# Kernel tuning notes

Hardware: AMD Instinct MI355X
Metric: run time of the kernel (lower is better)

The kernel has to match this reference:

```python
import jax, jax.numpy as jnp
import numpy as np
from jax.ops import segment_sum

N_NODES = 50000
N_EDGES = 800000
NUM_FEAT = 16
EDGE_DIM = 8
H = 100
L = 2
BN_EPS = 1e-5


def setup_inputs() -> dict:
    key = jax.random.key(0)
    ks = iter(jax.random.split(key, 40))
    def w(shape, scale=0.05):
        return (jax.random.normal(next(ks), shape, dtype=jnp.float32) * scale)
    inp = {
        "x": jax.random.normal(next(ks), (N_NODES, NUM_FEAT), dtype=jnp.float32),
        "edge_index": jax.random.randint(next(ks), (2, N_EDGES), 0, N_NODES, dtype=jnp.int64) if jax.config.jax_enable_x64 else jax.random.randint(next(ks), (2, N_EDGES), 0, N_NODES).astype(jnp.int32),
        "edge_attr": jax.random.normal(next(ks), (N_EDGES, EDGE_DIM), dtype=jnp.float32),
        # embeddings
        "node_w": w((NUM_FEAT, H)), "node_b": w((H,)),
        "edge_w": w((EDGE_DIM, H)), "edge_b": w((H,)),
        # per-layer GINEConv MLP (stacked over layers)
        "conv_w1": w((L, H, H)), "conv_b1": w((L, H)),
        "conv_w2": w((L, H, H)), "conv_b2": w((L, H)),
        # batchnorm affine params
        "bn_gamma": jnp.ones((L, H), dtype=jnp.float32), "bn_beta": jnp.zeros((L, H), dtype=jnp.float32),
        # per-layer edge-update MLP
        "emlp_w1": w((L, 3 * H, H)), "emlp_b1": w((L, H)),
        "emlp_w2": w((L, H, H)), "emlp_b2": w((L, H)),
        # final classifier MLP (3H -> 50 -> 25 -> 2); dropout is identity at eval
        "mlp_w1": w((3 * H, 50)), "mlp_b1": w((50,)),
        "mlp_w2": w((50, 25)), "mlp_b2": w((25,)),
        "mlp_w3": w((25, 2)), "mlp_b3": w((2,)),
    }
    return inp


def reference(x, edge_index, edge_attr,
              node_w, node_b, edge_w, edge_b,
              conv_w1, conv_b1, conv_w2, conv_b2,
              bn_gamma, bn_beta,
              emlp_w1, emlp_b1, emlp_w2, emlp_b2,
              mlp_w1, mlp_b1, mlp_w2, mlp_b2, mlp_w3, mlp_b3):
    src, dst = edge_index[0], edge_index[1]
    n_nodes = x.shape[0]

    h = x @ node_w + node_b          # [N, H]
    e = edge_attr @ edge_w + edge_b  # [E, H]

    for i in range(L):
        # GINEConv: out_i = nn((1+eps)*h_i + sum_{e: dst=i} relu(h_src + e)); eps=0
        msg = jax.nn.relu(h[src] + e)                       # [E, H] gather + combine
        agg = segment_sum(msg, dst, num_segments=n_nodes)   # [N, H] scatter-add
        z = h + agg
        z = jax.nn.relu(z @ conv_w1[i] + conv_b1[i]) @ conv_w2[i] + conv_b2[i]
        # BatchNorm (train mode: batch stats over nodes, biased variance)
        mu = jnp.mean(z, axis=0)
        var = jnp.var(z, axis=0)
        z = (z - mu) * jax.lax.rsqrt(var + BN_EPS) * bn_gamma[i] + bn_beta[i]
        h = (h + jax.nn.relu(z)) * 0.5
        # edge update: e += MLP([h_src, h_dst, e]) / 2
        cat = jnp.concatenate([h[src], h[dst], e], axis=-1)  # [E, 3H]
        upd = jax.nn.relu(cat @ emlp_w1[i] + emlp_b1[i]) @ emlp_w2[i] + emlp_b2[i]
        e = e + upd * 0.5

    # per-edge features: relu([h_src, h_dst]) ++ e  -> [E, 3H]
    feat = jnp.concatenate([jax.nn.relu(jnp.concatenate([h[src], h[dst]], axis=-1)), e], axis=-1)
    out = jax.nn.relu(feat @ mlp_w1 + mlp_b1)
    out = jax.nn.relu(out @ mlp_w2 + mlp_b2)
    return out @ mlp_w3 + mlp_b3  # [E, 2]
```

## Files before the change

kernel.cpp:

```cpp
#include <hip/hip_runtime.h>
#include <hip/hip_bf16.h>

#define N_NODES 50000
#define N_EDGES 800000
#define HDIM 100
#define ESTR 104

typedef _Float16 half8_t __attribute__((ext_vector_type(8)));
typedef float f32x4_t __attribute__((ext_vector_type(4)));

struct FragDesc {
  const float* src; int stride; int K; int N; int outOff; int ksteps; int ntiles;
};
struct PrepArgs {
  FragDesc d[17];
  int prefix[18];
  int ndesc;
};

__global__ void k_prep_frags(PrepArgs args, _Float16* __restrict__ out) {
  int b = blockIdx.x;
  int di = 0;
  while (di + 1 < args.ndesc && b >= args.prefix[di + 1]) di++;
  FragDesc d = args.d[di];
  int local = b - args.prefix[di];
  int t = local / d.ksteps;
  int s = local % d.ksteps;
  int lane = threadIdx.x;
  int col = t * 16 + (lane & 15);
  int kb = s * 32 + (lane >> 4) * 8;
  _Float16* o = out + d.outOff + (size_t)((t * d.ksteps + s) * 64 + lane) * 8;
  #pragma unroll
  for (int i = 0; i < 8; ++i) {
    int k = kb + i;
    float v = (k < d.K && col < d.N) ? d.src[(size_t)k * d.stride + col] : 0.0f;
    o[i] = (_Float16)v;
  }
}

__global__ void k_ws_probe(float* out, float mb) { out[0] = mb; }

__device__ __forceinline__ half8_t h8_zero() {
  half8_t a;
  #pragma unroll
  for (int i = 0; i < 8; ++i) a[i] = (_Float16)0.0f;
  return a;
}

__device__ __forceinline__ int swz_idx(int r, int c) {
  int chunk = (c >> 3) ^ (r & 7);
  return r * 128 + chunk * 8 + (c & 7);
}

template<int MODE>
__device__ __forceinline__ void load_a_node(const float* hp0,
                                            const float* ap0,
                                            int row, int lane, half8_t av[4]) {
  int g = lane >> 4;
  bool rv = (row < N_NODES);
  const float* hp = hp0 + (size_t)row * HDIM;
  const float* ap = ap0 + (size_t)row * HDIM;
  #pragma unroll
  for (int s = 0; s < 4; ++s) {
    int kb = s * 32 + g * 8;
    half8_t a = h8_zero();
    if (rv && kb < HDIM) {
      float f[8];
      #pragma unroll
      for (int i = 0; i < 8; ++i) f[i] = 0.0f;
      if (kb + 8 <= HDIM) {
        float4 v0 = *(const float4*)(hp + kb);
        float4 v1 = *(const float4*)(hp + kb + 4);
        f[0] = v0.x; f[1] = v0.y; f[2] = v0.z; f[3] = v0.w;
        f[4] = v1.x; f[5] = v1.y; f[6] = v1.z; f[7] = v1.w;
        if constexpr (MODE == 2) {
          float4 u0 = *(const float4*)(ap + kb);
          float4 u1 = *(const float4*)(ap + kb + 4);
          f[0] += u0.x; f[1] += u0.y; f[2] += u0.z; f[3] += u0.w;
          f[4] += u1.x; f[5] += u1.y; f[6] += u1.z; f[7] += u1.w;
        }
      } else {
        float4 v0 = *(const float4*)(hp + kb);
        f[0] = v0.x; f[1] = v0.y; f[2] = v0.z; f[3] = v0.w;
        if constexpr (MODE == 2) {
          float4 u0 = *(const float4*)(ap + kb);
          f[0] += u0.x; f[1] += u0.y; f[2] += u0.z; f[3] += u0.w;
        }
      }
      #pragma unroll
      for (int i = 0; i < 8; ++i) {
        float v = f[i];
        if constexpr (MODE == 1) v = fmaxf(v, 0.0f);
        a[i] = (_Float16)v;
      }
    }
    av[s] = a;
  }
}

template<int NT, int KS>
__device__ __forceinline__ void mfma_tiles(const half8_t* av, const _Float16* __restrict__ fb,
                                           int lane, f32x4_t* acc) {
  #pragma unroll
  for (int t = 0; t < NT; ++t) {
    #pragma unroll
    for (int s = 0; s < KS; ++s) {
      half8_t bv = *(const half8_t*)(fb + (size_t)(((t * KS + s) * 64 + lane) << 3));
      acc[t] = __builtin_amdgcn_mfma_f32_16x16x32_f16(av[s], bv, acc[t], 0, 0, 0);
    }
  }
}

template<int KS>
__device__ __forceinline__ void lds_read_a(const _Float16* L, int lane, half8_t* av) {
  int r = lane & 15;
  int g = lane >> 4;
  #pragma unroll
  for (int s = 0; s < KS; ++s) {
    int kb = s * 32 + g * 8;
    av[s] = *(const half8_t*)&L[swz_idx(r, kb)];
  }
}

__global__ void k_embed_h(const float* __restrict__ x, const float* __restrict__ w,
                          const float* __restrict__ bias, float* __restrict__ h) {
  int n = blockIdx.x;
  int j = threadIdx.x;
  if (j >= HDIM) return;
  float acc = bias[j];
  #pragma unroll
  for (int k = 0; k < 16; ++k) acc += x[n * 16 + k] * w[k * HDIM + j];
  h[(size_t)n * HDIM + j] = acc;
}

__global__ void k_embed_e(const float* __restrict__ attr, const float* __restrict__ w,
                          const float* __restrict__ bias, const int* __restrict__ src,
                          const int* __restrict__ dst, const float* __restrict__ h,
                          _Float16* __restrict__ e, float* __restrict__ agg) {
  int tid = threadIdx.x;
  int edge = blockIdx.x * 2 + (tid >> 7);
  int j = tid & 127;
  if (edge >= N_EDGES || j >= ESTR) return;
  float acc = 0.0f;
  if (j < HDIM) {
    acc = bias[j];
    #pragma unroll
    for (int k = 0; k < 8; ++k) acc += attr[edge * 8 + k] * w[k * HDIM + j];
  }
  e[(size_t)edge * ESTR + j] = (_Float16)acc;
  if (j < HDIM) {
    float m = h[(size_t)src[edge] * HDIM + j] + acc;
    if (m > 0.0f) atomicAdd(&agg[(size_t)dst[edge] * HDIM + j], m);
  }
}

__global__ __launch_bounds__(256) void k_node_conv(
    const float* __restrict__ h, const float* agg,
    const _Float16* __restrict__ fb1, const _Float16* __restrict__ fb2,
    const float* __restrict__ b1, const float* __restrict__ b2,
    float* z, float* __restrict__ bn_sum, float* __restrict__ bn_sq) {
  __shared__ __align__(16) _Float16 lds[4][2048];
  int lane = threadIdx.x & 63;
  int wave = threadIdx.x >> 6;
  _Float16* L = lds[wave];
  int mbase = (blockIdx.x * 4 + wave) * 16;

  half8_t av[4];
  load_a_node<2>(h, agg, mbase + (lane & 15), lane, av);
  f32x4_t acc[7];
  #pragma unroll
  for (int t = 0; t < 7; ++t) acc[t] = (f32x4_t){0.f, 0.f, 0.f, 0.f};
  mfma_tiles<7, 4>(av, fb1, lane, acc);

  #pragma unroll
  for (int t = 0; t < 7; ++t) {
    int j = t * 16 + (lane & 15);
    float bias = (j < HDIM) ? b1[j] : 0.0f;
    #pragma unroll
    for (int q = 0; q < 4; ++q) {
      int r = (lane >> 4) * 4 + q;
      float v = fmaxf(acc[t][q] + bias, 0.0f);
      if (j >= HDIM) v = 0.0f;
      L[swz_idx(r, j)] = (_Float16)v;
    }
  }
  {
    int r = lane >> 2; int c0 = 112 + (lane & 3) * 4;
    #pragma unroll
    for (int i = 0; i < 4; ++i) L[swz_idx(r, c0 + i)] = (_Float16)0.0f;
  }
  __builtin_amdgcn_sched_barrier(0);

  half8_t av2[4];
  lds_read_a<4>(L, lane, av2);
  f32x4_t acc2[7];
  #pragma unroll
  for (int t = 0; t < 7; ++t) acc2[t] = (f32x4_t){0.f, 0.f, 0.f, 0.f};
  mfma_tiles<7, 4>(av2, fb2, lane, acc2);
  __builtin_amdgcn_sched_barrier(0);

  #pragma unroll
  for (int t = 0; t < 7; ++t) {
    int j = t * 16 + (lane & 15);
    float bias = (j < HDIM) ? b2[j] : 0.0f;
    float colsum = 0.0f, colsq = 0.0f;
    #pragma unroll
    for (int q = 0; q < 4; ++q) {
      int row = mbase + (lane >> 4) * 4 + q;
      float v = acc2[t][q] + bias;
      bool ok = (row < N_NODES) && (j < HDIM);
      if (ok) z[(size_t)row * HDIM + j] = v;
      float sv = ok ? v : 0.0f;
      colsum += sv; colsq += sv * sv;
    }
    colsum += __shfl_xor(colsum, 16);
    colsum += __shfl_xor(colsum, 32);
    colsq  += __shfl_xor(colsq, 16);
    colsq  += __shfl_xor(colsq, 32);
    if (lane < 16 && j < HDIM) {
      atomicAdd(&bn_sum[j], colsum);
      atomicAdd(&bn_sq[j], colsq);
    }
  }
}

__global__ void k_bn_final(const float* __restrict__ bn_sum, const float* __restrict__ bn_sq,
                           float* __restrict__ bn_mu, float* __restrict__ bn_rs) {
  int j = threadIdx.x;
  if (j >= HDIM) return;
  float mu = bn_sum[j] / (float)N_NODES;
  float var = bn_sq[j] / (float)N_NODES - mu * mu;
  bn_mu[j] = mu;
  bn_rs[j] = rsqrtf(var + 1e-5f);
}

__global__ void k_h_update(float* __restrict__ h, const float* __restrict__ z,
                           const float* __restrict__ bn_mu, const float* __restrict__ bn_rs,
                           const float* __restrict__ gamma, const float* __restrict__ beta) {
  int idx = blockIdx.x * blockDim.x + threadIdx.x;
  if (idx >= N_NODES * HDIM) return;
  int j = idx % HDIM;
  float zn = (z[idx] - bn_mu[j]) * bn_rs[j] * gamma[j] + beta[j];
  h[idx] = 0.5f * (h[idx] + fmaxf(zn, 0.0f));
}

template<int NT, bool RELU, int OSTRIDE>
__global__ __launch_bounds__(256) void k_node_gemm(const float* __restrict__ h,
                                                   const _Float16* __restrict__ fb,
                                                   _Float16* __restrict__ out) {
  int lane = threadIdx.x & 63;
  int wave = threadIdx.x >> 6;
  int mbase = (blockIdx.x * 4 + wave) * 16;
  half8_t av[4];
  load_a_node<RELU ? 1 : 0>(h, h, mbase + (lane & 15), lane, av);
  f32x4_t acc[NT];
  #pragma unroll
  for (int t = 0; t < NT; ++t) acc[t] = (f32x4_t){0.f, 0.f, 0.f, 0.f};
  mfma_tiles<NT, 4>(av, fb, lane, acc);
  #pragma unroll
  for (int t = 0; t < NT; ++t) {
    int j = t * 16 + (lane & 15);
    #pragma unroll
    for (int q = 0; q < 4; ++q) {
      int row = mbase + (lane >> 4) * 4 + q;
      if (row < N_NODES) out[(size_t)row * OSTRIDE + j] = (_Float16)acc[t][q];
    }
  }
}

template<bool CLASSIFY>
__global__ __launch_bounds__(256) void k_edge(
    _Float16* __restrict__ e, const float* __restrict__ h,
    const _Float16* __restrict__ PQ,
    const int* __restrict__ src, const int* __restrict__ dst,
    const _Float16* __restrict__ fbW1c, const _Float16* __restrict__ fbW2,
    const float* __restrict__ b1, const float* __restrict__ b2,
    float* __restrict__ agg,
    const _Float16* __restrict__ RS,
    const _Float16* __restrict__ fbC, const _Float16* __restrict__ fbM2,
    const _Float16* __restrict__ fbM3,
    const float* __restrict__ mb1, const float* __restrict__ mb2,
    const float* __restrict__ mb3,
    float* __restrict__ out) {
  __shared__ __align__(16) _Float16 lds[4][2048];
  int lane = threadIdx.x & 63;
  int wave = threadIdx.x >> 6;
  _Float16* L = lds[wave];
  int mbase = (blockIdx.x * 4 + wave) * 16;

  int sn[4], dn[4];
  #pragma unroll
  for (int q = 0; q < 4; ++q) {
    int row = mbase + (lane >> 4) * 4 + q;
    sn[q] = src[row]; dn[q] = dst[row];
  }

  half8_t av[4];
  {
    const _Float16* ep = e + (size_t)(mbase + (lane & 15)) * ESTR;
    int g = lane >> 4;
    #pragma unroll
    for (int s = 0; s < 3; ++s)
      av[s] = *(const half8_t*)(ep + s * 32 + g * 8);
    av[3] = (g == 0) ? *(const half8_t*)(ep + 96) : h8_zero();
  }
  f32x4_t acc[7];
  #pragma unroll
  for (int t = 0; t < 7; ++t) acc[t] = (f32x4_t){0.f, 0.f, 0.f, 0.f};
  mfma_tiles<7, 4>(av, fbW1c, lane, acc);

  #pragma unroll
  for (int t = 0; t < 7; ++t) {
    int j = t * 16 + (lane & 15);
    float bias = (j < HDIM) ? b1[j] : 0.0f;
    #pragma unroll
    for (int q = 0; q < 4; ++q) {
      int r = (lane >> 4) * 4 + q;
      float v = 0.0f;
      if (j < HDIM) {
        float pv = (float)PQ[(size_t)sn[q] * 224 + j];
        float qv = (float)PQ[(size_t)dn[q] * 224 + 112 + j];
        v = fmaxf(acc[t][q] + bias + pv + qv, 0.0f);
      }
      L[swz_idx(r, j)] = (_Float16)v;
    }
  }
  { int r = lane >> 2; int c0 = 112 + (lane & 3) * 4;
    #pragma unroll
    for (int i = 0; i < 4; ++i) L[swz_idx(r, c0 + i)] = (_Float16)0.0f;
  }
  __builtin_amdgcn_sched_barrier(0);

  half8_t av2[4];
  lds_read_a<4>(L, lane, av2);
  f32x4_t acc2[7];
  #pragma unroll
  for (int t = 0; t < 7; ++t) acc2[t] = (f32x4_t){0.f, 0.f, 0.f, 0.f};
  mfma_tiles<7, 4>(av2, fbW2, lane, acc2);
  __builtin_amdgcn_sched_barrier(0);

  #pragma unroll
  for (int t = 0; t < 7; ++t) {
    int j = t * 16 + (lane & 15);
    float bias = (j < HDIM) ? b2[j] : 0.0f;
    #pragma unroll
    for (int q = 0; q < 4; ++q) {
      int row = mbase + (lane >> 4) * 4 + q;
      float upd = acc2[t][q] + bias;
      float enew = 0.0f;
      if (j < HDIM) {
        float eold = (float)e[(size_t)row * ESTR + j];
        enew = eold + 0.5f * upd;
      }
      if constexpr (!CLASSIFY) {
        if (j < HDIM) {
          e[(size_t)row * ESTR + j] = (_Float16)enew;
          float m = h[(size_t)sn[q] * HDIM + j] + enew;
          if (m > 0.0f) atomicAdd(&agg[(size_t)dn[q] * HDIM + j], m);
        }
      } else {
        int r = (lane >> 4) * 4 + q;
        L[swz_idx(r, j)] = (_Float16)((j < HDIM) ? enew : 0.0f);
      }
    }
  }

  if constexpr (CLASSIFY) {
    __builtin_amdgcn_sched_barrier(0);
    half8_t av3[4];
    lds_read_a<4>(L, lane, av3);
    f32x4_t acc3[4];
    #pragma unroll
    for (int t = 0; t < 4; ++t) acc3[t] = (f32x4_t){0.f, 0.f, 0.f, 0.f};
    mfma_tiles<4, 4>(av3, fbC, lane, acc3);
    __builtin_amdgcn_sched_barrier(0);
    #pragma unroll
    for (int t = 0; t < 4; ++t) {
      int j = t * 16 + (lane & 15);
      float bias = (j < 50) ? mb1[j] : 0.0f;
      #pragma unroll
      for (int q = 0; q < 4; ++q) {
        float v = 0.0f;
        if (j < 50) {
          float rv = (float)RS[(size_t)sn[q] * 128 + j];
          float sv = (float)RS[(size_t)dn[q] * 128 + 64 + j];
          v = fmaxf(acc3[t][q] + bias + rv + sv, 0.0f);
        }
        int r = (lane >> 4) * 4 + q;
        L[swz_idx(r, j)] = (_Float16)v;
      }
    }
    __builtin_amdgcn_sched_barrier(0);
    half8_t av4[2];
    lds_read_a<2>(L, lane, av4);
    f32x4_t acc4[2];
    #pragma unroll
    for (int t = 0; t < 2; ++t) acc4[t] = (f32x4_t){0.f, 0.f, 0.f, 0.f};
    mfma_tiles<2, 2>(av4, fbM2, lane, acc4);
    __builtin_amdgcn_sched_barrier(0);
    #pragma unroll
    for (int t = 0; t < 2; ++t) {
      int j = t * 16 + (lane & 15);
      float bias = (j < 25) ? mb2[j] : 0.0f;
      #pragma unroll
      for (int q = 0; q < 4; ++q) {
        float v = (j < 25) ? fmaxf(acc4[t][q] + bias, 0.0f) : 0.0f;
        int r = (lane >> 4) * 4 + q;
        L[swz_idx(r, j)] = (_Float16)v;
      }
    }
    __builtin_amdgcn_sched_barrier(0);
    half8_t av5[1];
    lds_read_a<1>(L, lane, av5);
    f32x4_t acc5 = (f32x4_t){0.f, 0.f, 0.f, 0.f};
    {
      half8_t bv = *(const half8_t*)(fbM3 + (size_t)(lane << 3));
      acc5 = __builtin_amdgcn_mfma_f32_16x16x32_f16(av5[0], bv, acc5, 0, 0, 0);
    }
    int j5 = lane & 15;
    if (j5 < 2) {
      float bias = mb3[j5];
      #pragma unroll
      for (int q = 0; q < 4; ++q) {
        int row = mbase + (lane >> 4) * 4 + q;
        out[(size_t)row * 2 + j5] = acc5[q] + bias;
      }
    }
  }
}

extern "C" void kernel_launch(void* const* d_in, const int* in_sizes, int n_in,
                              void* d_out, int out_size, void* d_ws, size_t ws_size,
                              hipStream_t stream) {
  const float* x        = (const float*)d_in[0];
  const int*   ei       = (const int*)  d_in[1];
  const float* eattr    = (const float*)d_in[2];
  const float* node_w   = (const float*)d_in[3];
  const float* node_b   = (const float*)d_in[4];
  const float* edge_w   = (const float*)d_in[5];
  const float* edge_b   = (const float*)d_in[6];
  const float* conv_w1  = (const float*)d_in[7];
  const float* conv_b1  = (const float*)d_in[8];
  const float* conv_w2  = (const float*)d_in[9];
  const float* conv_b2  = (const float*)d_in[10];
  const float* bn_gamma = (const float*)d_in[11];
  const float* bn_beta  = (const float*)d_in[12];
  const float* emlp_w1  = (const float*)d_in[13];
  const float* emlp_b1  = (const float*)d_in[14];
  const float* emlp_w2  = (const float*)d_in[15];
  const float* emlp_b2  = (const float*)d_in[16];
  const float* mlp_w1   = (const float*)d_in[17];
  const float* mlp_b1   = (const float*)d_in[18];
  const float* mlp_w2   = (const float*)d_in[19];
  const float* mlp_b2   = (const float*)d_in[20];
  const float* mlp_w3   = (const float*)d_in[21];
  const float* mlp_b3   = (const float*)d_in[22];
  const int* src = ei;
  const int* dst = ei + N_EDGES;

  char* ws = (char*)d_ws;
  size_t off = 0;
  auto alloc = [&](size_t bytes) -> void* {
    void* p = ws + off;
    off += (bytes + 255) & ~(size_t)255;
    return p;
  };
  _Float16* e    = (_Float16*)alloc((size_t)N_EDGES * ESTR * 2);
  float* h       = (float*)alloc((size_t)N_NODES * HDIM * 4);
  float* agg     = (float*)alloc((size_t)N_NODES * HDIM * 4);
  _Float16* PQ   = (_Float16*)alloc((size_t)N_NODES * 224 * 2);
  _Float16* RS   = (_Float16*)alloc((size_t)N_NODES * 128 * 2);
  float* bn_sum  = (float*)alloc(512);
  float* bn_sq   = (float*)alloc(512);
  float* bn_mu   = (float*)alloc(512);
  float* bn_rs   = (float*)alloc(512);
  _Float16* frags = (_Float16*)alloc(220000 * 2);
  float* z = agg;

  if (off > ws_size) {
    k_ws_probe<<<1, 1, 0, stream>>>((float*)d_out, (float)(ws_size >> 20));
    return;
  }

  PrepArgs pa;
  int nd = 0, tilesum = 0, fo = 0;
  auto add = [&](const float* sp, int stride, int K, int Ncols, int ksteps, int ntiles) -> int {
    pa.d[nd] = FragDesc{sp, stride, K, Ncols, fo, ksteps, ntiles};
    pa.prefix[nd] = tilesum;
    tilesum += ksteps * ntiles;
    ++nd;
    int ret = fo;
    fo += ksteps * ntiles * 512;
    return ret;
  };
  int offConvW1[2], offConvW2[2], offPQ[2], offW1c[2], offW2e[2];
  for (int i = 0; i < 2; ++i) {
    offConvW1[i] = add(conv_w1 + i * 10000, 100, 100, 100, 4, 7);
    offConvW2[i] = add(conv_w2 + i * 10000, 100, 100, 100, 4, 7);
    offPQ[i]     = add(emlp_w1 + i * 30000,         100, 100, 100, 4, 7);
                   add(emlp_w1 + i * 30000 + 10000, 100, 100, 100, 4, 7);
    offW1c[i]    = add(emlp_w1 + i * 30000 + 20000, 100, 100, 100, 4, 7);
    offW2e[i]    = add(emlp_w2 + i * 10000, 100, 100, 100, 4, 7);
  }
  int offRS = add(mlp_w1,         50, 100, 50, 4, 4);
              add(mlp_w1 + 5000,  50, 100, 50, 4, 4);
  int offC  = add(mlp_w1 + 10000, 50, 100, 50, 4, 4);
  int offM2 = add(mlp_w2, 25, 50, 25, 2, 2);
  int offM3 = add(mlp_w3, 2, 25, 2, 1, 1);
  pa.prefix[nd] = tilesum;
  pa.ndesc = nd;

  const size_t aggBytes = (size_t)N_NODES * HDIM * 4;

  hipMemsetAsync(agg, 0, aggBytes, stream);
  k_prep_frags<<<tilesum, 64, 0, stream>>>(pa, frags);
  k_embed_h<<<N_NODES, 128, 0, stream>>>(x, node_w, node_b, h);
  k_embed_e<<<N_EDGES / 2, 256, 0, stream>>>(eattr, edge_w, edge_b, src, dst, h, e, agg);

  const int nodeGrid = (N_NODES + 63) / 64;
  for (int i = 0; i < 2; ++i) {
    hipMemsetAsync(bn_sum, 0, 512, stream);
    hipMemsetAsync(bn_sq, 0, 512, stream);
    k_node_conv<<<nodeGrid, 256, 0, stream>>>(h, agg, frags + offConvW1[i], frags + offConvW2[i],
                                              conv_b1 + i * 100, conv_b2 + i * 100,
                                              z, bn_sum, bn_sq);
    k_bn_final<<<1, 128, 0, stream>>>(bn_sum, bn_sq, bn_mu, bn_rs);
    k_h_update<<<(N_NODES * HDIM + 255) / 256, 256, 0, stream>>>(h, z, bn_mu, bn_rs,
                                                                 bn_gamma + i * 100, bn_beta + i * 100);
    k_node_gemm<14, false, 224><<<nodeGrid, 256, 0, stream>>>(h, frags + offPQ[i], PQ);
    if (i == 0) {
      hipMemsetAsync(agg, 0, aggBytes, stream);
      k_edge<false><<<N_EDGES / 64, 256, 0, stream>>>(
          e, h, PQ, src, dst, frags + offW1c[0], frags + offW2e[0],
          emlp_b1, emlp_b2, agg,
          nullptr, nullptr, nullptr, nullptr, nullptr, nullptr, nullptr, nullptr);
    } else {
      k_node_gemm<8, true, 128><<<nodeGrid, 256, 0, stream>>>(h, frags + offRS, RS);
      k_edge<true><<<N_EDGES / 64, 256, 0, stream>>>(
          e, h, PQ, src, dst, frags + offW1c[1], frags + offW2e[1],
          emlp_b1 + 100, emlp_b2 + 100, nullptr,
          RS, frags + offC, frags + offM2, frags + offM3,
          mlp_b1, mlp_b2, mlp_b3, (float*)d_out);
    }
  }
}
```

Baseline: 1.685 ms.

## Store node projections in fragment-transposed layout for vectorized edge gathers

The node GEMM now writes the P/Q and R/S projections in a lane-major layout, so each lane's values for all its output tiles are contiguous. The edge kernel can then fetch them with one 16-byte (or 8-byte) vector load per source and destination node, prefetched early, instead of many scattered scalar half loads inside the epilogue loop. The RS buffer now reuses the agg workspace. This trades padded storage (256 vs 224 halves per node) and extra live registers for far fewer gather instructions.

```diff
diff --git a/kernel.cpp b/kernel.cpp
--- a/kernel.cpp
+++ b/kernel.cpp
@@ -7,14 +7,15 @@
 #define ESTR 104
 
 typedef _Float16 half8_t __attribute__((ext_vector_type(8)));
+typedef _Float16 half4_t __attribute__((ext_vector_type(4)));
 typedef float f32x4_t __attribute__((ext_vector_type(4)));
 
 struct FragDesc {
   const float* src; int stride; int K; int N; int outOff; int ksteps; int ntiles;
 };
 struct PrepArgs {
-  FragDesc d[17];
-  int prefix[18];
+  FragDesc d[20];
+  int prefix[21];
   int ndesc;
 };
 
@@ -145,7 +146,7 @@
   if (j < HDIM) {
     acc = bias[j];
     #pragma unroll
-    for (int k = 0; k < 8; ++k) acc += attr[edge * 8 + k] * w[k * HDIM + j];
+    for (int k = 0; k < 8; ++k) acc += attr[(size_t)edge * 8 + k] * w[k * HDIM + j];
   }
   e[(size_t)edge * ESTR + j] = (_Float16)acc;
   if (j < HDIM) {
@@ -244,26 +245,43 @@
   h[idx] = 0.5f * (h[idx] + fmaxf(zn, 0.0f));
 }
 
-template<int NT, bool RELU, int OSTRIDE>
-__global__ __launch_bounds__(256) void k_node_gemm(const float* __restrict__ h,
-                                                   const _Float16* __restrict__ fb,
-                                                   _Float16* __restrict__ out) {
+template<bool RS>
+__global__ __launch_bounds__(256) void k_node_gemm_t(const float* __restrict__ h,
+                                                     const _Float16* __restrict__ fb,
+                                                     _Float16* __restrict__ out) {
+  constexpr int NT = RS ? 8 : 14;
   int lane = threadIdx.x & 63;
   int wave = threadIdx.x >> 6;
+  int c = lane & 15;
   int mbase = (blockIdx.x * 4 + wave) * 16;
   half8_t av[4];
-  load_a_node<RELU ? 1 : 0>(h, h, mbase + (lane & 15), lane, av);
+  load_a_node<RS ? 1 : 0>(h, h, mbase + c, lane, av);
   f32x4_t acc[NT];
   #pragma unroll
   for (int t = 0; t < NT; ++t) acc[t] = (f32x4_t){0.f, 0.f, 0.f, 0.f};
   mfma_tiles<NT, 4>(av, fb, lane, acc);
   #pragma unroll
-  for (int t = 0; t < NT; ++t) {
-    int j = t * 16 + (lane & 15);
-    #pragma unroll
-    for (int q = 0; q < 4; ++q) {
-      int row = mbase + (lane >> 4) * 4 + q;
-      if (row < N_NODES) out[(size_t)row * OSTRIDE + j] = (_Float16)acc[t][q];
+  for (int q = 0; q < 4; ++q) {
+    int row = mbase + (lane >> 4) * 4 + q;
+    if (row >= N_NODES) continue;
+    if constexpr (!RS) {
+      half8_t hp, hq;
+      #pragma unroll
+      for (int t = 0; t < 8; ++t) {
+        hp[t] = (t < 7) ? (_Float16)acc[t][q] : (_Float16)0.0f;
+        hq[t] = (t < 7) ? (_Float16)acc[7 + t][q] : (_Float16)0.0f;
+      }
+      *(half8_t*)(out + (size_t)row * 256 + c * 8) = hp;
+      *(half8_t*)(out + (size_t)row * 256 + 128 + c * 8) = hq;
+    } else {
+      half4_t hr, hs;
+      #pragma unroll
+      for (int t = 0; t < 4; ++t) {
+        hr[t] = (_Float16)acc[t][q];
+        hs[t] = (_Float16)acc[4 + t][q];
+      }
+      *(half4_t*)(out + (size_t)row * 128 + c * 4) = hr;
+      *(half4_t*)(out + (size_t)row * 128 + 64 + c * 4) = hs;
     }
   }
 }
@@ -287,18 +305,25 @@
   int wave = threadIdx.x >> 6;
   _Float16* L = lds[wave];
   int mbase = (blockIdx.x * 4 + wave) * 16;
+  int c = lane & 15, g = lane >> 4;
 
   int sn[4], dn[4];
   #pragma unroll
   for (int q = 0; q < 4; ++q) {
-    int row = mbase + (lane >> 4) * 4 + q;
+    int row = mbase + g * 4 + q;
     sn[q] = src[row]; dn[q] = dst[row];
+  }
+
+  half8_t Pf[4], Qf[4];
+  #pragma unroll
+  for (int q = 0; q < 4; ++q) {
+    Pf[q] = *(const half8_t*)(PQ + (size_t)sn[q] * 256 + c * 8);
+    Qf[q] = *(const half8_t*)(PQ + (size_t)dn[q] * 256 + 128 + c * 8);
   }
 
   half8_t av[4];
   {
-    const _Float16* ep = e + (size_t)(mbase + (lane & 15)) * ESTR;
-    int g = lane >> 4;
+    const _Float16* ep = e + (size_t)(mbase + c) * ESTR;
     #pragma unroll
     for (int s = 0; s < 3; ++s)
       av[s] = *(const half8_t*)(ep + s * 32 + g * 8);
@@ -311,17 +336,14 @@
 
   #pragma unroll
   for (int t = 0; t < 7; ++t) {
-    int j = t * 16 + (lane & 15);
+    int j = t * 16 + c;
     float bias = (j < HDIM) ? b1[j] : 0.0f;
     #pragma unroll
     for (int q = 0; q < 4; ++q) {
-      int r = (lane >> 4) * 4 + q;
+      int r = g * 4 + q;
       float v = 0.0f;
-      if (j < HDIM) {
-        float pv = (float)PQ[(size_t)sn[q] * 224 + j];
-        float qv = (float)PQ[(size_t)dn[q] * 224 + 112 + j];
-        v = fmaxf(acc[t][q] + bias + pv + qv, 0.0f);
-      }
+      if (j < HDIM)
+        v = fmaxf(acc[t][q] + bias + (float)Pf[q][t] + (float)Qf[q][t], 0.0f);
       L[swz_idx(r, j)] = (_Float16)v;
     }
   }
@@ -330,6 +352,15 @@
     for (int i = 0; i < 4; ++i) L[swz_idx(r, c0 + i)] = (_Float16)0.0f;
   }
   __builtin_amdgcn_sched_barrier(0);
+
+  half4_t Rf[4], Sf[4];
+  if constexpr (CLASSIFY) {
+    #pragma unroll
+    for (int q = 0; q < 4; ++q) {
+      Rf[q] = *(const half4_t*)(RS + (size_t)sn[q] * 128 + c * 4);
+      Sf[q] = *(const half4_t*)(RS + (size_t)dn[q] * 128 + 64 + c * 4);
+    }
+  }
 
   half8_t av2[4];
   lds_read_a<4>(L, lane, av2);
@@ -341,11 +372,11 @@
 
   #pragma unroll
   for (int t = 0; t < 7; ++t) {
-    int j = t * 16 + (lane & 15);
+    int j = t * 16 + c;
     float bias = (j < HDIM) ? b2[j] : 0.0f;
     #pragma unroll
     for (int q = 0; q < 4; ++q) {
-      int row = mbase + (lane >> 4) * 4 + q;
+      int row = mbase + g * 4 + q;
       float upd = acc2[t][q] + bias;
       float enew = 0.0f;
       if (j < HDIM) {
@@ -359,7 +390,7 @@
           if (m > 0.0f) atomicAdd(&agg[(size_t)dn[q] * HDIM + j], m);
         }
       } else {
-        int r = (lane >> 4) * 4 + q;
+        int r = g * 4 + q;
         L[swz_idx(r, j)] = (_Float16)((j < HDIM) ? enew : 0.0f);
       }
     }
@@ -376,17 +407,14 @@
     __builtin_amdgcn_sched_barrier(0);
     #pragma unroll
     for (int t = 0; t < 4; ++t) {
-      int j = t * 16 + (lane & 15);
+      int j = t * 16 + c;
       float bias = (j < 50) ? mb1[j] : 0.0f;
       #pragma unroll
       for (int q = 0; q < 4; ++q) {
         float v = 0.0f;
-        if (j < 50) {
-          float rv = (float)RS[(size_t)sn[q] * 128 + j];
-          float sv = (float)RS[(size_t)dn[q] * 128 + 64 + j];
-          v = fmaxf(acc3[t][q] + bias + rv + sv, 0.0f);
-        }
-        int r = (lane >> 4) * 4 + q;
+        if (j < 50)
+          v = fmaxf(acc3[t][q] + bias + (float)Rf[q][t] + (float)Sf[q][t], 0.0f);
+        int r = g * 4 + q;
         L[swz_idx(r, j)] = (_Float16)v;
       }
     }
@@ -400,12 +428,12 @@
     __builtin_amdgcn_sched_barrier(0);
     #pragma unroll
     for (int t = 0; t < 2; ++t) {
-      int j = t * 16 + (lane & 15);
+      int j = t * 16 + c;
       float bias = (j < 25) ? mb2[j] : 0.0f;
       #pragma unroll
       for (int q = 0; q < 4; ++q) {
         float v = (j < 25) ? fmaxf(acc4[t][q] + bias, 0.0f) : 0.0f;
-        int r = (lane >> 4) * 4 + q;
+        int r = g * 4 + q;
         L[swz_idx(r, j)] = (_Float16)v;
       }
     }
@@ -417,13 +445,12 @@
       half8_t bv = *(const half8_t*)(fbM3 + (size_t)(lane << 3));
       acc5 = __builtin_amdgcn_mfma_f32_16x16x32_f16(av5[0], bv, acc5, 0, 0, 0);
     }
-    int j5 = lane & 15;
-    if (j5 < 2) {
-      float bias = mb3[j5];
+    if (c < 2) {
+      float bias = mb3[c];
       #pragma unroll
       for (int q = 0; q < 4; ++q) {
-        int row = mbase + (lane >> 4) * 4 + q;
-        out[(size_t)row * 2 + j5] = acc5[q] + bias;
+        int row = mbase + g * 4 + q;
+        out[(size_t)row * 2 + c] = acc5[q] + bias;
       }
     }
   }
@@ -468,14 +495,14 @@
   _Float16* e    = (_Float16*)alloc((size_t)N_EDGES * ESTR * 2);
   float* h       = (float*)alloc((size_t)N_NODES * HDIM * 4);
   float* agg     = (float*)alloc((size_t)N_NODES * HDIM * 4);
-  _Float16* PQ   = (_Float16*)alloc((size_t)N_NODES * 224 * 2);
-  _Float16* RS   = (_Float16*)alloc((size_t)N_NODES * 128 * 2);
+  _Float16* PQt  = (_Float16*)alloc((size_t)N_NODES * 256 * 2);
   float* bn_sum  = (float*)alloc(512);
   float* bn_sq   = (float*)alloc(512);
   float* bn_mu   = (float*)alloc(512);
   float* bn_rs   = (float*)alloc(512);
-  _Float16* frags = (_Float16*)alloc(220000 * 2);
+  _Float16* frags = (_Float16*)alloc(200000 * 2);
   float* z = agg;
+  _Float16* RSt = (_Float16*)agg;
 
   if (off > ws_size) {
     k_ws_probe<<<1, 1, 0, stream>>>((float*)d_out, (float)(ws_size >> 20));
@@ -527,19 +554,19 @@
     k_bn_final<<<1, 128, 0, stream>>>(bn_sum, bn_sq, bn_mu, bn_rs);
     k_h_update<<<(N_NODES * HDIM + 255) / 256, 256, 0, stream>>>(h, z, bn_mu, bn_rs,
                                                                  bn_gamma + i * 100, bn_beta + i * 100);
-    k_node_gemm<14, false, 224><<<nodeGrid, 256, 0, stream>>>(h, frags + offPQ[i], PQ);
+    k_node_gemm_t<false><<<nodeGrid, 256, 0, stream>>>(h, frags + offPQ[i], PQt);
     if (i == 0) {
       hipMemsetAsync(agg, 0, aggBytes, stream);
       k_edge<false><<<N_EDGES / 64, 256, 0, stream>>>(
-          e, h, PQ, src, dst, frags + offW1c[0], frags + offW2e[0],
+          e, h, PQt, src, dst, frags + offW1c[0], frags + offW2e[0],
           emlp_b1, emlp_b2, agg,
           nullptr, nullptr, nullptr, nullptr, nullptr, nullptr, nullptr, nullptr);
     } else {
-      k_node_gemm<8, true, 128><<<nodeGrid, 256, 0, stream>>>(h, frags + offRS, RS);
+      k_node_gemm_t<true><<<nodeGrid, 256, 0, stream>>>(h, frags + offRS, RSt);
       k_edge<true><<<N_EDGES / 64, 256, 0, stream>>>(
-          e, h, PQ, src, dst, frags + offW1c[1], frags + offW2e[1],
+          e, h, PQt, src, dst, frags + offW1c[1], frags + offW2e[1],
           emlp_b1 + 100, emlp_b2 + 100, nullptr,
-          RS, frags + offC, frags + offM2, frags + offM3,
+          RSt, frags + offC, frags + offM2, frags + offM3,
           mlp_b1, mlp_b2, mlp_b3, (float*)d_out);
     }
   }
```

Result: no change. 1.688 ms (+0.2%).
